# Optimization experiments

Hardware: AMD Instinct MI355X
Metric: run time of the kernel (lower is better)

The kernel has to match this reference:

```python
import jax, jax.numpy as jnp
import numpy as np

B, C, H, W = 4, 128, 64, 64
CQ = C // 8  # query/key channels = 16


def setup_inputs() -> dict:
    key = jax.random.key(0)
    ks = jax.random.split(key, 8)
    s = 0.05
    return {
        "x": jax.random.normal(ks[0], (B, C, H, W), jnp.float32),
        "wq": jax.random.normal(ks[1], (CQ, C), jnp.float32) * s,
        "bq": jax.random.normal(ks[2], (CQ,), jnp.float32) * s,
        "wk": jax.random.normal(ks[3], (CQ, C), jnp.float32) * s,
        "bk": jax.random.normal(ks[4], (CQ,), jnp.float32) * s,
        "wv": jax.random.normal(ks[5], (C, C), jnp.float32) * s,
        "bv": jax.random.normal(ks[6], (C,), jnp.float32) * s,
        # original inits gamma to 0; use small nonzero so attention path is exercised
        "gamma": jax.random.normal(ks[7], (1,), jnp.float32) * 0.1,
    }


def reference(x, wq, bq, wk, bk, wv, bv, gamma):
    b, c, h, w = x.shape
    n = h * w
    xf = x.reshape(b, c, n)  # [B, C, N]
    # 1x1 convs are per-position linear maps over channels
    q = jnp.einsum("qc,bcn->bnq", wq, xf) + bq            # [B, N, Cq]
    k = jnp.einsum("qc,bcn->bqn", wk, xf) + bk[:, None]   # [B, Cq, N]
    v = jnp.einsum("oc,bcn->bon", wv, xf) + bv[:, None]   # [B, C, N]
    # unscaled scores, softmax over keys (last dim), as in the original
    attn = jax.nn.softmax(jnp.einsum("bnq,bqm->bnm", q, k), axis=-1)  # [B, N, N]
    # out = value @ attention^T : out[b,c,n] = sum_m v[b,c,m] * attn[b,n,m]
    out = jnp.einsum("bom,bnm->bon", v, attn)             # [B, C, N]
    return gamma[0] * out.reshape(b, c, h, w) + x
```

## Files before the change

kernel.cpp:

```cpp
#include <hip/hip_runtime.h>
#include <hip/hip_bf16.h>

typedef float f32x4  __attribute__((ext_vector_type(4)));
typedef float f32x16 __attribute__((ext_vector_type(16)));
typedef short s16x8  __attribute__((ext_vector_type(8)));

#define NB 4
#define NC 128
#define NNPOS 4096
#define KSP 8
#define LOG2E 1.44269504088896f

__device__ __forceinline__ short bf16s(float x) {
    __hip_bfloat16 h = __float2bfloat16(x);
    return *reinterpret_cast<short*>(&h);
}
__device__ __forceinline__ int packbf2(float lo, float hi) {
    __hip_bfloat162 t = __float22bfloat162_rn(float2{lo, hi});
    return *reinterpret_cast<int*>(&t);
}
__device__ __forceinline__ float bf2f(unsigned short u) {
    unsigned int v = ((unsigned int)u) << 16;
    return *reinterpret_cast<float*>(&v);
}
__device__ __forceinline__ float exp2fast(float x) {
    return __builtin_amdgcn_exp2f(x);
}

__global__ __launch_bounds__(256) void qkv_kernel(
    const float* __restrict__ x,
    const float* __restrict__ wq, const float* __restrict__ bq,
    const float* __restrict__ wk, const float* __restrict__ bk,
    const float* __restrict__ wv, const float* __restrict__ bv,
    short* __restrict__ qb, short* __restrict__ kb, short* __restrict__ vt)
{
    const int n0  = blockIdx.x * 32;
    const int b   = blockIdx.y;
    const int tid = threadIdx.x;
    const int w = tid >> 6, lane = tid & 63, quad = lane >> 4, nn = lane & 15;

    __shared__ __align__(16) short xsT[32 * 136];

    #pragma unroll
    for (int p = 0; p < 4; ++p) {
        int idx = tid + p * 256;
        int cc = idx >> 3, n4 = (idx & 7) * 4;
        f32x4 xv = *(const f32x4*)&x[((size_t)(b * NC + cc)) * NNPOS + n0 + n4];
        #pragma unroll
        for (int j = 0; j < 4; ++j)
            xsT[(n4 + j) * 136 + cc] = bf16s(xv[j]);
    }

    s16x8 af[3][4];
    bool  live[3];
    f32x4 biasv[3];
    #pragma unroll
    for (int t = 0; t < 3; ++t) {
        int rid = 3 * w + t;
        int R   = rid * 16;
        const float* wsrc = nullptr; const float* bsrc = nullptr; int row0 = 0;
        float scale = 1.0f;
        if (rid < 8)        { wsrc = wv; bsrc = bv; row0 = R; }
        else if (rid == 8)  { wsrc = wq; bsrc = bq; row0 = 0; scale = LOG2E; }
        else if (rid == 10) { wsrc = wk; bsrc = bk; row0 = 0; }
        live[t] = (wsrc != nullptr);
        #pragma unroll
        for (int r = 0; r < 4; ++r)
            biasv[t][r] = live[t] ? scale * bsrc[row0 + quad * 4 + r] : 0.0f;
        if (live[t]) {
            #pragma unroll
            for (int ks = 0; ks < 4; ++ks) {
                const float* src = wsrc + (size_t)(row0 + nn) * NC + ks * 32 + quad * 8;
                f32x4 wa = *(const f32x4*)src;
                f32x4 wb = *(const f32x4*)(src + 4);
                s16x8 f;
                #pragma unroll
                for (int j = 0; j < 4; ++j) {
                    f[j]     = bf16s(scale * wa[j]);
                    f[j + 4] = bf16s(scale * wb[j]);
                }
                af[t][ks] = f;
            }
        }
    }
    __syncthreads();

    f32x4 acc[3][2];
    #pragma unroll
    for (int t = 0; t < 3; ++t)
        #pragma unroll
        for (int nt = 0; nt < 2; ++nt)
            acc[t][nt] = biasv[t];

    #pragma unroll
    for (int nt = 0; nt < 2; ++nt) {
        s16x8 bf[4];
        #pragma unroll
        for (int ks = 0; ks < 4; ++ks)
            bf[ks] = *(const s16x8*)&xsT[(nt * 16 + nn) * 136 + ks * 32 + quad * 8];
        #pragma unroll
        for (int t = 0; t < 3; ++t)
            if (live[t])
                #pragma unroll
                for (int ks = 0; ks < 4; ++ks)
                    acc[t][nt] = __builtin_amdgcn_mfma_f32_16x16x32_bf16(af[t][ks], bf[ks], acc[t][nt], 0, 0, 0);
    }

    #pragma unroll
    for (int t = 0; t < 3; ++t) {
        if (!live[t]) continue;
        int R = (3 * w + t) * 16;
        #pragma unroll
        for (int nt = 0; nt < 2; ++nt) {
            int n = n0 + nt * 16 + nn;
            int kg = (n0 + nt * 16) >> 4;
            #pragma unroll
            for (int r = 0; r < 4; ++r) {
                short v = bf16s(acc[t][nt][r]);
                int row = R + quad * 4 + r;
                if (row < 128) {
                    int ct = row >> 5, c31r = row & 31;
                    vt[((((size_t)b * 256 + kg) * 4 + ct) * 32 + c31r) * 16 + nn] = v;
                } else if (row < 144)
                    qb[((size_t)(b * NNPOS) + n) * 16 + (row - 128)] = v;
                else
                    kb[((size_t)(b * NNPOS) + n) * 16 + (row - 160)] = v;
            }
        }
    }
}

__global__ __launch_bounds__(256, 2) void attn_kernel(
    const short* __restrict__ qb, const short* __restrict__ kb,
    const short* __restrict__ vt,
    unsigned short* __restrict__ Ow, float* __restrict__ lw)
{
    const int s   = blockIdx.x;
    const int b   = blockIdx.z;
    const int tid = threadIdx.x;
    const int w = tid >> 6, lane = tid & 63, h = lane >> 5, c31 = lane & 31;

    const int qt = blockIdx.y * 4 + w;
    const int q0 = qt * 32;

    s16x8 bq = *(const s16x8*)(qb + ((size_t)(b * NNPOS) + q0 + c31) * 16 + h * 8);

    f32x16 acc[4];
    #pragma unroll
    for (int ct = 0; ct < 4; ++ct)
        #pragma unroll
        for (int r = 0; r < 16; ++r) acc[ct][r] = 0.0f;
    float lp = 0.0f;

    const short* kbp = kb + (size_t)(b * NNPOS) * 16;
    const short* vbp = vt + (size_t)b * (256 * 4 * 512);
    const int mbase = s * (NNPOS / KSP);
    const int kgbase = mbase >> 4;

    #pragma unroll 2
    for (int it = 0; it < (NNPOS / KSP) / 64; ++it) {
        const int m0 = mbase + it * 64;
        const int kg0 = kgbase + it * 4;

        s16x8 ak0 = *(const s16x8*)(kbp + (size_t)(m0      + c31) * 16 + h * 8);
        s16x8 ak1 = *(const s16x8*)(kbp + (size_t)(m0 + 32 + c31) * 16 + h * 8);

        s16x8 vb[4][4];
        #pragma unroll
        for (int kp = 0; kp < 4; ++kp)
            #pragma unroll
            for (int ct = 0; ct < 4; ++ct)
                vb[kp][ct] = *(const s16x8*)(vbp +
                    (((size_t)(kg0 + kp) * 4 + ct) << 9) + (c31 << 4) + (h << 3));

        f32x16 z;
        #pragma unroll
        for (int r = 0; r < 16; ++r) z[r] = 0.0f;
        f32x16 s0 = __builtin_amdgcn_mfma_f32_32x32x16_bf16(ak0, bq, z, 0, 0, 0);
        f32x16 s1 = __builtin_amdgcn_mfma_f32_32x32x16_bf16(ak1, bq, z, 0, 0, 0);

        int d[16];
        #pragma unroll
        for (int i = 0; i < 8; ++i) {
            float p0 = exp2fast(fminf(s0[2 * i], 126.f));
            float p1 = exp2fast(fminf(s0[2 * i + 1], 126.f));
            lp += p0 + p1;
            d[i] = packbf2(p0, p1);
        }
        #pragma unroll
        for (int i = 0; i < 8; ++i) {
            float p0 = exp2fast(fminf(s1[2 * i], 126.f));
            float p1 = exp2fast(fminf(s1[2 * i + 1], 126.f));
            lp += p0 + p1;
            d[8 + i] = packbf2(p0, p1);
        }
        int xw[16];
        #pragma unroll
        for (int i = 0; i < 16; ++i) xw[i] = __shfl_xor(d[i], 32, 64);

        s16x8 pa[4];
        #pragma unroll
        for (int kp = 0; kp < 4; ++kp) {
            int e = kp * 4;
            union { int i[4]; s16x8 v; } u;
            u.i[0] = h ? xw[e + 2] : d[e];
            u.i[1] = h ? xw[e + 3] : d[e + 1];
            u.i[2] = h ? d[e + 2]  : xw[e];
            u.i[3] = h ? d[e + 3]  : xw[e + 1];
            pa[kp] = u.v;
        }

        #pragma unroll
        for (int kp = 0; kp < 4; ++kp)
            #pragma unroll
            for (int ct = 0; ct < 4; ++ct)
                acc[ct] = __builtin_amdgcn_mfma_f32_32x32x16_bf16(
                    pa[kp], vb[kp][ct], acc[ct], 0, 0, 0);
    }

    lp += __shfl_xor(lp, 32, 64);
    if (lane < 32)
        lw[((size_t)(b * KSP + s)) * NNPOS + q0 + c31] = lp;

    #pragma unroll
    for (int ct = 0; ct < 4; ++ct)
        #pragma unroll
        for (int r = 0; r < 16; ++r) {
            int q = q0 + (r & 3) + 8 * (r >> 2) + 4 * h;
            Ow[(((size_t)(b * KSP + s)) * NNPOS + q) * NC + ct * 32 + c31] =
                (unsigned short)bf16s(acc[ct][r]);
        }
}

__global__ __launch_bounds__(256) void combine_kernel(
    const unsigned short* __restrict__ Ow, const float* __restrict__ lw,
    const float* __restrict__ x, const float* __restrict__ gamma,
    float* __restrict__ out)
{
    const int n0  = blockIdx.x * 64;
    const int b   = blockIdx.y;
    const int tid = threadIdx.x;

    __shared__ float ot[128 * 65 + 64];
    float* lsum = ot + 128 * 65;

    if (tid < 64) {
        float sl = 0.f;
        #pragma unroll
        for (int sI = 0; sI < KSP; ++sI)
            sl += lw[((size_t)(b * KSP + sI)) * NNPOS + n0 + tid];
        lsum[tid] = sl;
    }
    __syncthreads();

    #pragma unroll
    for (int p = 0; p < 16; ++p) {
        int e = tid + p * 256;
        int cp = e & 63, n = e >> 6;
        float a0 = 0.f, a1 = 0.f;
        #pragma unroll
        for (int sI = 0; sI < KSP; ++sI) {
            const unsigned short* src = Ow +
                (((size_t)(b * KSP + sI)) * NNPOS + n0 + n) * NC + cp * 2;
            ushort2 u = *(const ushort2*)src;
            a0 += bf2f(u.x);
            a1 += bf2f(u.y);
        }
        float inv = 1.0f / lsum[n];
        ot[(cp * 2) * 65 + n]     = a0 * inv;
        ot[(cp * 2 + 1) * 65 + n] = a1 * inv;
    }
    __syncthreads();

    const float g = gamma[0];
    #pragma unroll
    for (int p = 0; p < 32; ++p) {
        int e = tid + p * 256;
        int n = e & 63, c = e >> 6;
        size_t a = ((size_t)(b * NC + c)) * NNPOS + n0 + n;
        out[a] = g * ot[c * 65 + n] + x[a];
    }
}

extern "C" void kernel_launch(void* const* d_in, const int* in_sizes, int n_in,
                              void* d_out, int out_size, void* d_ws, size_t ws_size,
                              hipStream_t stream) {
    const float* x     = (const float*)d_in[0];
    const float* wq    = (const float*)d_in[1];
    const float* bq    = (const float*)d_in[2];
    const float* wk    = (const float*)d_in[3];
    const float* bk    = (const float*)d_in[4];
    const float* wv    = (const float*)d_in[5];
    const float* bv    = (const float*)d_in[6];
    const float* gamma = (const float*)d_in[7];
    float* out = (float*)d_out;

    short* qb = (short*)d_ws;
    short* kb = qb + (size_t)NB * NNPOS * 16;
    short* vt = kb + (size_t)NB * NNPOS * 16;
    unsigned short* Ow = (unsigned short*)(vt + (size_t)NB * NC * NNPOS);
    float* lw = (float*)(Ow + (size_t)NB * KSP * NNPOS * NC);

    qkv_kernel<<<dim3(128, NB), 256, 0, stream>>>(x, wq, bq, wk, bk, wv, bv, qb, kb, vt);
    attn_kernel<<<dim3(KSP, 32, NB), 256, 0, stream>>>(qb, kb, vt, Ow, lw);
    combine_kernel<<<dim3(NNPOS / 64, NB), 256, 0, stream>>>(Ow, lw, x, gamma, out);
}
```

Before: 127.0 us.

## Halve key splits, double-buffer V loads, raise occupancy, widen combine loads

Halves the key-dimension split from 8 to 4, which cuts partial-output traffic and combine work but doubles the per-block loop length and halves grid parallelism. The attention loop now interleaves softmax exponentiation with MFMA per key sub-block and double-buffers V fragment loads instead of loading all 16 up front. This lowers register pressure so launch bounds can ask for 3 blocks per CU. It also removes the fminf clamp before exp2, which risks overflow for large scores. The combine kernel switches to 4-wide bf16 loads.

```diff
diff --git a/kernel.cpp b/kernel.cpp
--- a/kernel.cpp
+++ b/kernel.cpp
@@ -8,7 +8,7 @@
 #define NB 4
 #define NC 128
 #define NNPOS 4096
-#define KSP 8
+#define KSP 4
 #define LOG2E 1.44269504088896f
 
 __device__ __forceinline__ short bf16s(float x) {
@@ -130,7 +130,7 @@
     }
 }
 
-__global__ __launch_bounds__(256, 2) void attn_kernel(
+__global__ __launch_bounds__(256, 3) void attn_kernel(
     const short* __restrict__ qb, const short* __restrict__ kb,
     const short* __restrict__ vt,
     unsigned short* __restrict__ Ow, float* __restrict__ lw)
@@ -157,7 +157,6 @@
     const int mbase = s * (NNPOS / KSP);
     const int kgbase = mbase >> 4;
 
-    #pragma unroll 2
     for (int it = 0; it < (NNPOS / KSP) / 64; ++it) {
         const int m0 = mbase + it * 64;
         const int kg0 = kgbase + it * 4;
@@ -165,13 +164,11 @@
         s16x8 ak0 = *(const s16x8*)(kbp + (size_t)(m0      + c31) * 16 + h * 8);
         s16x8 ak1 = *(const s16x8*)(kbp + (size_t)(m0 + 32 + c31) * 16 + h * 8);
 
-        s16x8 vb[4][4];
-        #pragma unroll
-        for (int kp = 0; kp < 4; ++kp)
-            #pragma unroll
-            for (int ct = 0; ct < 4; ++ct)
-                vb[kp][ct] = *(const s16x8*)(vbp +
-                    (((size_t)(kg0 + kp) * 4 + ct) << 9) + (c31 << 4) + (h << 3));
+        s16x8 vbuf[2][4];
+        #pragma unroll
+        for (int ct = 0; ct < 4; ++ct)
+            vbuf[0][ct] = *(const s16x8*)(vbp +
+                (((size_t)kg0 * 4 + ct) << 9) + (c31 << 4) + (h << 3));
 
         f32x16 z;
         #pragma unroll
@@ -179,43 +176,37 @@
         f32x16 s0 = __builtin_amdgcn_mfma_f32_32x32x16_bf16(ak0, bq, z, 0, 0, 0);
         f32x16 s1 = __builtin_amdgcn_mfma_f32_32x32x16_bf16(ak1, bq, z, 0, 0, 0);
 
-        int d[16];
-        #pragma unroll
-        for (int i = 0; i < 8; ++i) {
-            float p0 = exp2fast(fminf(s0[2 * i], 126.f));
-            float p1 = exp2fast(fminf(s0[2 * i + 1], 126.f));
-            lp += p0 + p1;
-            d[i] = packbf2(p0, p1);
-        }
-        #pragma unroll
-        for (int i = 0; i < 8; ++i) {
-            float p0 = exp2fast(fminf(s1[2 * i], 126.f));
-            float p1 = exp2fast(fminf(s1[2 * i + 1], 126.f));
-            lp += p0 + p1;
-            d[8 + i] = packbf2(p0, p1);
-        }
-        int xw[16];
-        #pragma unroll
-        for (int i = 0; i < 16; ++i) xw[i] = __shfl_xor(d[i], 32, 64);
-
-        s16x8 pa[4];
         #pragma unroll
         for (int kp = 0; kp < 4; ++kp) {
-            int e = kp * 4;
+            if (kp < 3) {
+                #pragma unroll
+                for (int ct = 0; ct < 4; ++ct)
+                    vbuf[(kp + 1) & 1][ct] = *(const s16x8*)(vbp +
+                        (((size_t)(kg0 + kp + 1) * 4 + ct) << 9) + (c31 << 4) + (h << 3));
+            }
+            const int off = (kp & 1) * 8;
+            int d[4], xw[4];
+            #pragma unroll
+            for (int i = 0; i < 4; ++i) {
+                float sa = (kp < 2) ? s0[off + 2 * i]     : s1[off + 2 * i];
+                float sb = (kp < 2) ? s0[off + 2 * i + 1] : s1[off + 2 * i + 1];
+                float p0 = exp2fast(sa);
+                float p1 = exp2fast(sb);
+                lp += p0 + p1;
+                d[i] = packbf2(p0, p1);
+            }
+            #pragma unroll
+            for (int i = 0; i < 4; ++i) xw[i] = __shfl_xor(d[i], 32, 64);
             union { int i[4]; s16x8 v; } u;
-            u.i[0] = h ? xw[e + 2] : d[e];
-            u.i[1] = h ? xw[e + 3] : d[e + 1];
-            u.i[2] = h ? d[e + 2]  : xw[e];
-            u.i[3] = h ? d[e + 3]  : xw[e + 1];
-            pa[kp] = u.v;
-        }
-
-        #pragma unroll
-        for (int kp = 0; kp < 4; ++kp)
+            u.i[0] = h ? xw[2] : d[0];
+            u.i[1] = h ? xw[3] : d[1];
+            u.i[2] = h ? d[2]  : xw[0];
+            u.i[3] = h ? d[3]  : xw[1];
             #pragma unroll
             for (int ct = 0; ct < 4; ++ct)
                 acc[ct] = __builtin_amdgcn_mfma_f32_32x32x16_bf16(
-                    pa[kp], vb[kp][ct], acc[ct], 0, 0, 0);
+                    u.v, vbuf[kp & 1][ct], acc[ct], 0, 0, 0);
+        }
     }
 
     lp += __shfl_xor(lp, 32, 64);
@@ -254,21 +245,22 @@
     __syncthreads();
 
     #pragma unroll
-    for (int p = 0; p < 16; ++p) {
+    for (int p = 0; p < 8; ++p) {
         int e = tid + p * 256;
-        int cp = e & 63, n = e >> 6;
-        float a0 = 0.f, a1 = 0.f;
+        int cq = e & 31, n = e >> 5;
+        float a0 = 0.f, a1 = 0.f, a2 = 0.f, a3 = 0.f;
         #pragma unroll
         for (int sI = 0; sI < KSP; ++sI) {
             const unsigned short* src = Ow +
-                (((size_t)(b * KSP + sI)) * NNPOS + n0 + n) * NC + cp * 2;
-            ushort2 u = *(const ushort2*)src;
-            a0 += bf2f(u.x);
-            a1 += bf2f(u.y);
+                (((size_t)(b * KSP + sI)) * NNPOS + n0 + n) * NC + cq * 4;
+            ushort4 u = *(const ushort4*)src;
+            a0 += bf2f(u.x); a1 += bf2f(u.y); a2 += bf2f(u.z); a3 += bf2f(u.w);
         }
         float inv = 1.0f / lsum[n];
-        ot[(cp * 2) * 65 + n]     = a0 * inv;
-        ot[(cp * 2 + 1) * 65 + n] = a1 * inv;
+        ot[(cq * 4) * 65 + n]     = a0 * inv;
+        ot[(cq * 4 + 1) * 65 + n] = a1 * inv;
+        ot[(cq * 4 + 2) * 65 + n] = a2 * inv;
+        ot[(cq * 4 + 3) * 65 + n] = a3 * inv;
     }
     __syncthreads();
 
```

Result: slower. 168.5 us (+32.6%).
